# Optimization experiments

Measured on AMD Instinct MI355X. Metric: run time of the kernel, lower is better.

The kernel has to match this reference:

```python
import jax, jax.numpy as jnp
import numpy as np


def setup_inputs() -> dict:
    key = jax.random.key(0)
    ks = jax.random.split(key, 5)
    B, H, S, C, Dh = 2, 16, 2048, 2048, 64
    HID = H * Dh
    return {
        "q": jax.random.normal(ks[0], (B, H, S, Dh), dtype=jnp.float32),
        "k": jax.random.normal(ks[1], (B, H, C + S, Dh), dtype=jnp.float32),
        "v": jax.random.normal(ks[2], (B, H, C + S, Dh), dtype=jnp.float32),
        "memory_length": 256,
        "W": jax.random.normal(ks[3], (HID, HID), dtype=jnp.float32) / np.sqrt(HID),
        "b": jax.random.normal(ks[4], (HID,), dtype=jnp.float32) * 0.01,
    }


def _build_mask(S, KV, memory_length):
    # KV = CACHE_LEN + S; columns >= CACHE_LEN + memory_length are restricted.
    C = KV - S
    rows = jnp.arange(S)[:, None]          # query position in [0, S)
    cols = jnp.arange(KV)[None, :]         # key position in [0, KV)
    restricted = cols >= (C + memory_length)
    # memory rows (< memory_length) never see restricted cols;
    # other rows: strictly-upper-triangular masking (col - (C+mem) > row - mem)
    mem_row = rows < memory_length
    future = (cols - (C + memory_length)) > (rows - memory_length)
    return (restricted & (mem_row | future))  # bool [S, KV], True = masked


def reference(q, k, v, memory_length, W, b):
    B, H, S, Dh = q.shape
    KV = k.shape[2]
    HID = H * Dh
    scale = 1.0 / np.sqrt(Dh).astype(np.float32)
    scores = jnp.einsum('bhsd,bhtd->bhst', q, k) * scale   # [B,H,S,KV]
    mask2d = _build_mask(S, KV, memory_length)             # [S,KV] bool
    scores = jnp.where(mask2d[None, None], -jnp.inf, scores)
    attn_w = jax.nn.softmax(scores, axis=-1)
    attn = jnp.einsum('bhst,bhtd->bshd', attn_w, v).reshape(B, S, HID)
    out = attn @ W.T + b
    # torch module returns full [B,H,S,KV] float mask of 0/1
    mask_full = jnp.broadcast_to(mask2d.astype(q.dtype), (B, H, S, KV))
    return out, mask_full
```

## Files before the change

kernel.cpp:

```cpp
#include <hip/hip_runtime.h>
#include <hip/hip_bf16.h>
#include <math.h>

typedef __bf16 bf16;
typedef __bf16 bf16x4 __attribute__((ext_vector_type(4)));
typedef __bf16 bf16x8 __attribute__((ext_vector_type(8)));
typedef float f32x4 __attribute__((ext_vector_type(4)));

#define MFMA(a, b, c) __builtin_amdgcn_mfma_f32_16x16x32_bf16((a), (b), (c), 0, 0, 0)

constexpr int Bb  = 2;
constexpr int Hh  = 16;
constexpr int Ss  = 2048;
constexpr int KVv = 4096;
constexpr int Dd  = 64;
constexpr int Cc  = KVv - Ss;
constexpr int HID = Hh * Dd;

constexpr float QSCL = 0.125f * 1.44269504088896340736f;

constexpr size_t MASK_F4   = (size_t)Bb * Hh * Ss * KVv / 4;
constexpr size_t SCR_BYTES = 16777216ull + 16777216ull + 2097152ull + 8388608ull;
constexpr size_t M2_F4     = MASK_F4 - (2097152ull + 8388608ull) / 16;
constexpr size_t M1_F4     = 50000000;

__device__ __forceinline__ void write_mask_range(
    float* __restrict__ mout, int mem, size_t lo, size_t hi,
    int mblk, int nmblk, int tid, int nthr)
{
    const int R = Cc + mem;
    const size_t stride = (size_t)nmblk * nthr;
    for (size_t i = lo + (size_t)mblk * nthr + tid; i < hi; i += stride) {
        size_t flat = i * 4;
        int t = (int)(flat & (size_t)(KVv - 1));
        int s = (int)((flat >> 12) & (size_t)(Ss - 1));
        int thr = (s < mem) ? R : (s + Cc + 1);
        f32x4 vv;
        vv[0] = (float)(t >= thr);
        vv[1] = (float)(t + 1 >= thr);
        vv[2] = (float)(t + 2 >= thr);
        vv[3] = (float)(t + 3 >= thr);
        __builtin_nontemporal_store(vv, (f32x4*)(mout + flat));
    }
}

__global__ __launch_bounds__(256) void cvt_kernel(
    const float* __restrict__ K, const float* __restrict__ W,
    bf16* __restrict__ Kb, bf16* __restrict__ Wb)
{
    const size_t nK4 = (size_t)Bb * Hh * KVv * Dd / 4;
    const size_t nW4 = (size_t)HID * HID / 4;
    const size_t total = nK4 + nW4;
    const size_t stride = (size_t)gridDim.x * blockDim.x;
    for (size_t i = (size_t)blockIdx.x * blockDim.x + threadIdx.x; i < total; i += stride) {
        float4 x = (i < nK4) ? ((const float4*)K)[i] : ((const float4*)W)[i - nK4];
        bf16x4 t;
        t[0] = (bf16)x.x; t[1] = (bf16)x.y; t[2] = (bf16)x.z; t[3] = (bf16)x.w;
        if (i < nK4) ((bf16x4*)Kb)[i] = t;
        else         ((bf16x4*)Wb)[i - nK4] = t;
    }
}

__global__ __launch_bounds__(256) void vT_kernel(
    const float* __restrict__ V, bf16* __restrict__ Vt)
{
    __shared__ __align__(16) bf16 T[64][72];
    const int bh = blockIdx.y;
    const int t0 = blockIdx.x * 64;
    const int row = threadIdx.x >> 2;
    const int cg  = threadIdx.x & 3;

    const float* vb = V + (size_t)bh * KVv * Dd + (size_t)(t0 + row) * Dd + cg * 16;
    float4 x0 = ((const float4*)vb)[0];
    float4 x1 = ((const float4*)vb)[1];
    float4 x2 = ((const float4*)vb)[2];
    float4 x3 = ((const float4*)vb)[3];
    float xs[16] = {x0.x,x0.y,x0.z,x0.w, x1.x,x1.y,x1.z,x1.w,
                    x2.x,x2.y,x2.z,x2.w, x3.x,x3.y,x3.z,x3.w};
#pragma unroll
    for (int j = 0; j < 16; ++j)
        T[cg * 16 + j][row] = (bf16)xs[j];
    __syncthreads();

    const int d = row;
    bf16* o = Vt + (size_t)bh * Dd * KVv + (size_t)d * KVv + t0 + cg * 16;
    bf16x8 a0 = *(const bf16x8*)&T[d][cg * 16];
    bf16x8 a1 = *(const bf16x8*)&T[d][cg * 16 + 8];
    ((bf16x8*)o)[0] = a0;
    ((bf16x8*)o)[1] = a1;
}

template <bool MASKED>
__device__ __forceinline__ void kv_tile(
    int t0, const bf16* __restrict__ kb_p, const bf16* __restrict__ vt_p,
    const bf16x8 qa[2], const int thr[4], int tid, int lr, int lg,
    bf16 (*__restrict__ Klds)[72], bf16 (*__restrict__ Vlds)[72],
    bf16 (*__restrict__ Pw)[72], f32x4 acco[4], float lsum[4])
{
    {
        const int row = tid >> 3, c8 = tid & 7;
        bf16x8 kx = *(const bf16x8*)(kb_p + (size_t)(t0 + row) * Dd + c8 * 8);
        bf16x8 vx = *(const bf16x8*)(vt_p + (size_t)row * KVv + t0 + c8 * 8);
        *(bf16x8*)&Klds[row][c8 * 8] = kx;
        *(bf16x8*)&Vlds[row][c8 * 8] = vx;
    }
    __syncthreads();

    f32x4 accs[4];
#pragma unroll
    for (int kg = 0; kg < 4; ++kg) accs[kg] = (f32x4){0.f, 0.f, 0.f, 0.f};
    __builtin_amdgcn_s_setprio(1);
#pragma unroll
    for (int ks = 0; ks < 2; ++ks) {
#pragma unroll
        for (int kg = 0; kg < 4; ++kg) {
            bf16x8 kf = *(const bf16x8*)&Klds[kg * 16 + lr][ks * 32 + lg * 8];
            accs[kg] = MFMA(qa[ks], kf, accs[kg]);
        }
    }
    __builtin_amdgcn_s_setprio(0);

#pragma unroll
    for (int r = 0; r < 4; ++r) {
#pragma unroll
        for (int kg = 0; kg < 4; ++kg) {
            float sl = accs[kg][r];
            if (MASKED) {
                int tcol = t0 + kg * 16 + lr;
                sl = (tcol < thr[r]) ? sl : -1e30f;
            }
            accs[kg][r] = __builtin_amdgcn_exp2f(sl);
        }
        lsum[r] += (accs[0][r] + accs[1][r]) + (accs[2][r] + accs[3][r]);
#pragma unroll
        for (int kg = 0; kg < 4; ++kg)
            Pw[lg * 4 + r][kg * 16 + lr] = (bf16)accs[kg][r];
    }
    asm volatile("s_waitcnt lgkmcnt(0)" ::: "memory");

    __builtin_amdgcn_s_setprio(1);
#pragma unroll
    for (int ks = 0; ks < 2; ++ks) {
        bf16x8 pa = *(const bf16x8*)&Pw[lr][ks * 32 + lg * 8];
#pragma unroll
        for (int dg = 0; dg < 4; ++dg) {
            bf16x8 vf = *(const bf16x8*)&Vlds[dg * 16 + lr][ks * 32 + lg * 8];
            acco[dg] = MFMA(pa, vf, acco[dg]);
        }
    }
    __builtin_amdgcn_s_setprio(0);
    __syncthreads();
}

__global__ __launch_bounds__(512) void fused_attn_kernel(
    const float* __restrict__ q, const bf16* __restrict__ Kb,
    const bf16* __restrict__ Vtb, const int* __restrict__ memp,
    bf16* __restrict__ attnb, float* __restrict__ mout)
{
    __shared__ __align__(16) bf16 Klds[64][72];
    __shared__ __align__(16) bf16 Vlds[64][72];
    __shared__ __align__(16) bf16 Plds[8][16][72];

    const int fid = blockIdx.x;
    const int mem = *memp;
    if (fid >= 512) {
        write_mask_range(mout, mem, 0, M1_F4, fid - 512, gridDim.x - 512,
                         threadIdx.x, 512);
        return;
    }
    const int xcd = fid & 7;
    const int slot = fid >> 3;
    const int qblk = slot & 15;
    const int bh = (slot >> 4) * 8 + xcd;

    const int tid = threadIdx.x;
    const int w  = tid >> 6;
    const int l  = tid & 63;
    const int lr = l & 15;
    const int lg = l >> 4;
    const int q0 = qblk * 128;
    const int R = Cc + mem;

    const float* qp   = q   + (size_t)bh * Ss * Dd;
    const bf16*  kb_p = Kb  + (size_t)bh * KVv * Dd;
    const bf16*  vt_p = Vtb + (size_t)bh * Dd * KVv;

    const int qrow = q0 + w * 16 + lr;
    bf16x8 qa[2];
#pragma unroll
    for (int ks = 0; ks < 2; ++ks) {
        const float* p8 = qp + (size_t)qrow * Dd + ks * 32 + lg * 8;
        float4 x0 = *(const float4*)p8;
        float4 x1 = *(const float4*)(p8 + 4);
        bf16x8 a;
        a[0] = (bf16)(x0.x * QSCL); a[1] = (bf16)(x0.y * QSCL);
        a[2] = (bf16)(x0.z * QSCL); a[3] = (bf16)(x0.w * QSCL);
        a[4] = (bf16)(x1.x * QSCL); a[5] = (bf16)(x1.y * QSCL);
        a[6] = (bf16)(x1.z * QSCL); a[7] = (bf16)(x1.w * QSCL);
        qa[ks] = a;
    }

    int thr[4];
#pragma unroll
    for (int r = 0; r < 4; ++r) {
        int qabs = q0 + w * 16 + lg * 4 + r;
        thr[r] = (qabs < mem) ? R : (qabs + Cc + 1);
    }
    const int qmaxb = q0 + 127;
    int kv_end = (qmaxb < mem) ? R : (qmaxb + Cc + 1);
    if (kv_end > KVv) kv_end = KVv;
    int thr_min = (q0 < mem) ? R : (q0 + Cc + 1);
    int p1_end = thr_min & ~63;
    if (p1_end > kv_end) p1_end = kv_end;

    f32x4 acco[4];
#pragma unroll
    for (int dg = 0; dg < 4; ++dg) acco[dg] = (f32x4){0.f, 0.f, 0.f, 0.f};
    float lsum[4] = {0.f, 0.f, 0.f, 0.f};

    for (int t0 = 0; t0 < p1_end; t0 += 64)
        kv_tile<false>(t0, kb_p, vt_p, qa, thr, tid, lr, lg, Klds, Vlds, Plds[w], acco, lsum);
    for (int t0 = p1_end; t0 < kv_end; t0 += 64)
        kv_tile<true>(t0, kb_p, vt_p, qa, thr, tid, lr, lg, Klds, Vlds, Plds[w], acco, lsum);

    const int b = bh >> 4, h = bh & 15;
#pragma unroll
    for (int r = 0; r < 4; ++r) {
        float s = lsum[r];
        s += __shfl_xor(s, 1);
        s += __shfl_xor(s, 2);
        s += __shfl_xor(s, 4);
        s += __shfl_xor(s, 8);
        float inv = 1.f / s;
        int qabs = q0 + w * 16 + lg * 4 + r;
        bf16* dst = attnb + (size_t)(b * Ss + qabs) * HID + h * Dd;
#pragma unroll
        for (int dg = 0; dg < 4; ++dg)
            dst[dg * 16 + lr] = (bf16)(acco[dg][r] * inv);
    }
}

__global__ __launch_bounds__(256) void fused_proj_kernel(
    const bf16* __restrict__ A, const bf16* __restrict__ Wb,
    const float* __restrict__ bias, float* __restrict__ out,
    const int* __restrict__ memp, float* __restrict__ mout)
{
    __shared__ __align__(16) bf16 Alds[64][72];
    __shared__ __align__(16) bf16 Wlds[64][72];

    const int fid = blockIdx.x;
    if (fid >= 1024) {
        write_mask_range(mout, *memp, M1_F4, M2_F4, fid - 1024, gridDim.x - 1024,
                         threadIdx.x, 256);
        return;
    }
    const int xcd = fid & 7;
    const int slot = fid >> 3;
    const int o0 = ((slot & 1) * 8 + xcd) * 64;
    const int i0 = (slot >> 1) * 64;

    const int tid = threadIdx.x;
    const int w  = tid >> 6;
    const int l  = tid & 63;
    const int lr = l & 15;
    const int lg = l >> 4;

    f32x4 acc[4];
#pragma unroll
    for (int og = 0; og < 4; ++og) acc[og] = (f32x4){0.f, 0.f, 0.f, 0.f};

    for (int kc = 0; kc < HID; kc += 64) {
        const int row = tid >> 2, cg = tid & 3;
        bf16x8 a0 = ((const bf16x8*)(A  + (size_t)(i0 + row) * HID + kc + cg * 16))[0];
        bf16x8 a1 = ((const bf16x8*)(A  + (size_t)(i0 + row) * HID + kc + cg * 16))[1];
        bf16x8 w0 = ((const bf16x8*)(Wb + (size_t)(o0 + row) * HID + kc + cg * 16))[0];
        bf16x8 w1 = ((const bf16x8*)(Wb + (size_t)(o0 + row) * HID + kc + cg * 16))[1];
        *(bf16x8*)&Alds[row][cg * 16]     = a0;
        *(bf16x8*)&Alds[row][cg * 16 + 8] = a1;
        *(bf16x8*)&Wlds[row][cg * 16]     = w0;
        *(bf16x8*)&Wlds[row][cg * 16 + 8] = w1;
        __syncthreads();
        __builtin_amdgcn_s_setprio(1);
#pragma unroll
        for (int ks = 0; ks < 2; ++ks) {
            bf16x8 af = *(const bf16x8*)&Alds[w * 16 + lr][ks * 32 + lg * 8];
#pragma unroll
            for (int og = 0; og < 4; ++og) {
                bf16x8 wf = *(const bf16x8*)&Wlds[og * 16 + lr][ks * 32 + lg * 8];
                acc[og] = MFMA(af, wf, acc[og]);
            }
        }
        __builtin_amdgcn_s_setprio(0);
        __syncthreads();
    }

#pragma unroll
    for (int r = 0; r < 4; ++r) {
        int i = i0 + w * 16 + lg * 4 + r;
#pragma unroll
        for (int og = 0; og < 4; ++og) {
            int o = o0 + og * 16 + lr;
            __builtin_nontemporal_store(acc[og][r] + bias[o], &out[(size_t)i * HID + o]);
        }
    }
}

__global__ __launch_bounds__(256) void mask_tail_kernel(
    float* __restrict__ mout, const int* __restrict__ memp)
{
    write_mask_range(mout, *memp, M2_F4, MASK_F4, blockIdx.x, gridDim.x,
                     threadIdx.x, 256);
}

extern "C" void kernel_launch(void* const* d_in, const int* in_sizes, int n_in,
                              void* d_out, int out_size, void* d_ws, size_t ws_size,
                              hipStream_t stream)
{
    (void)in_sizes; (void)n_in; (void)out_size; (void)d_ws; (void)ws_size;
    const float* q    = (const float*)d_in[0];
    const float* k    = (const float*)d_in[1];
    const float* v    = (const float*)d_in[2];
    const int*   memp = (const int*)d_in[3];
    const float* W    = (const float*)d_in[4];
    const float* bias = (const float*)d_in[5];

    float* out     = (float*)d_out;
    float* maskout = out + (size_t)Bb * Ss * HID;

    char* scr = (char*)maskout + MASK_F4 * 16 - SCR_BYTES;
    bf16* Kbf   = (bf16*)scr;
    bf16* Vtb   = Kbf + (size_t)Bb * Hh * KVv * Dd;
    bf16* Wbf   = Vtb + (size_t)Bb * Hh * KVv * Dd;
    bf16* attnb = Wbf + (size_t)HID * HID;

    cvt_kernel<<<dim3(1024), 256, 0, stream>>>(k, W, Kbf, Wbf);
    vT_kernel<<<dim3(KVv / 64, Bb * Hh), 256, 0, stream>>>(v, Vtb);
    fused_attn_kernel<<<dim3(512 + 1024), 512, 0, stream>>>(q, Kbf, Vtb, memp, attnb, maskout);
    fused_proj_kernel<<<dim3(1024 + 512), 256, 0, stream>>>(attnb, Wbf, bias, out, memp, maskout);
    mask_tail_kernel<<<dim3(256), 256, 0, stream>>>(maskout, memp);
}
```

Before: 265.9 us.

## Double query rows per attention block, merge prep kernels, use workspace scratch

Each attention block now handles 256 query rows (two 16-row subtiles per wave), so every K/V tile staged in LDS is reused twice and half as many blocks reload K/V. The V transpose and the K/W bf16 conversion are merged into one prep launch. When the workspace is large enough, scratch moves into it, so the mask tail can be written by the projection kernel and the separate tail launch is dropped. The mask split point is also retuned. The cost is doubled register use for accumulators and Q fragments, and fewer attention blocks.

After: 301.9 us. 1.14x slower.

```diff
diff --git a/kernel.cpp b/kernel.cpp
--- a/kernel.cpp
+++ b/kernel.cpp
@@ -22,7 +22,7 @@
 constexpr size_t MASK_F4   = (size_t)Bb * Hh * Ss * KVv / 4;
 constexpr size_t SCR_BYTES = 16777216ull + 16777216ull + 2097152ull + 8388608ull;
 constexpr size_t M2_F4     = MASK_F4 - (2097152ull + 8388608ull) / 16;
-constexpr size_t M1_F4     = 50000000;
+constexpr size_t M1_F4     = 40000000;
 
 __device__ __forceinline__ void write_mask_range(
     float* __restrict__ mout, int mem, size_t lo, size_t hi,
@@ -44,15 +44,40 @@
     }
 }
 
-__global__ __launch_bounds__(256) void cvt_kernel(
+__global__ __launch_bounds__(256) void prep_kernel(
     const float* __restrict__ K, const float* __restrict__ W,
-    bf16* __restrict__ Kb, bf16* __restrict__ Wb)
-{
+    const float* __restrict__ V,
+    bf16* __restrict__ Kb, bf16* __restrict__ Wb, bf16* __restrict__ Vt)
+{
+    const int bid = blockIdx.x;
+    if (bid < 2048) {
+        __shared__ __align__(16) bf16 T[64][72];
+        const int bh = bid >> 6;
+        const int t0 = (bid & 63) * 64;
+        const int row = threadIdx.x >> 2;
+        const int cg  = threadIdx.x & 3;
+        const float* vb = V + (size_t)bh * KVv * Dd + (size_t)(t0 + row) * Dd + cg * 16;
+        float4 x0 = ((const float4*)vb)[0];
+        float4 x1 = ((const float4*)vb)[1];
+        float4 x2 = ((const float4*)vb)[2];
+        float4 x3 = ((const float4*)vb)[3];
+        float xs[16] = {x0.x,x0.y,x0.z,x0.w, x1.x,x1.y,x1.z,x1.w,
+                        x2.x,x2.y,x2.z,x2.w, x3.x,x3.y,x3.z,x3.w};
+#pragma unroll
+        for (int j = 0; j < 16; ++j)
+            T[cg * 16 + j][row] = (bf16)xs[j];
+        __syncthreads();
+        const int d = row;
+        bf16* o = Vt + (size_t)bh * Dd * KVv + (size_t)d * KVv + t0 + cg * 16;
+        ((bf16x8*)o)[0] = *(const bf16x8*)&T[d][cg * 16];
+        ((bf16x8*)o)[1] = *(const bf16x8*)&T[d][cg * 16 + 8];
+        return;
+    }
     const size_t nK4 = (size_t)Bb * Hh * KVv * Dd / 4;
     const size_t nW4 = (size_t)HID * HID / 4;
     const size_t total = nK4 + nW4;
-    const size_t stride = (size_t)gridDim.x * blockDim.x;
-    for (size_t i = (size_t)blockIdx.x * blockDim.x + threadIdx.x; i < total; i += stride) {
+    const size_t stride = (size_t)(gridDim.x - 2048) * 256;
+    for (size_t i = (size_t)(bid - 2048) * 256 + threadIdx.x; i < total; i += stride) {
         float4 x = (i < nK4) ? ((const float4*)K)[i] : ((const float4*)W)[i - nK4];
         bf16x4 t;
         t[0] = (bf16)x.x; t[1] = (bf16)x.y; t[2] = (bf16)x.z; t[3] = (bf16)x.w;
@@ -61,41 +86,12 @@
     }
 }
 
-__global__ __launch_bounds__(256) void vT_kernel(
-    const float* __restrict__ V, bf16* __restrict__ Vt)
-{
-    __shared__ __align__(16) bf16 T[64][72];
-    const int bh = blockIdx.y;
-    const int t0 = blockIdx.x * 64;
-    const int row = threadIdx.x >> 2;
-    const int cg  = threadIdx.x & 3;
-
-    const float* vb = V + (size_t)bh * KVv * Dd + (size_t)(t0 + row) * Dd + cg * 16;
-    float4 x0 = ((const float4*)vb)[0];
-    float4 x1 = ((const float4*)vb)[1];
-    float4 x2 = ((const float4*)vb)[2];
-    float4 x3 = ((const float4*)vb)[3];
-    float xs[16] = {x0.x,x0.y,x0.z,x0.w, x1.x,x1.y,x1.z,x1.w,
-                    x2.x,x2.y,x2.z,x2.w, x3.x,x3.y,x3.z,x3.w};
-#pragma unroll
-    for (int j = 0; j < 16; ++j)
-        T[cg * 16 + j][row] = (bf16)xs[j];
-    __syncthreads();
-
-    const int d = row;
-    bf16* o = Vt + (size_t)bh * Dd * KVv + (size_t)d * KVv + t0 + cg * 16;
-    bf16x8 a0 = *(const bf16x8*)&T[d][cg * 16];
-    bf16x8 a1 = *(const bf16x8*)&T[d][cg * 16 + 8];
-    ((bf16x8*)o)[0] = a0;
-    ((bf16x8*)o)[1] = a1;
-}
-
 template <bool MASKED>
 __device__ __forceinline__ void kv_tile(
     int t0, const bf16* __restrict__ kb_p, const bf16* __restrict__ vt_p,
-    const bf16x8 qa[2], const int thr[4], int tid, int lr, int lg,
+    const bf16x8 qa[2][2], const int thr[2][4], int tid, int lr, int lg,
     bf16 (*__restrict__ Klds)[72], bf16 (*__restrict__ Vlds)[72],
-    bf16 (*__restrict__ Pw)[72], f32x4 acco[4], float lsum[4])
+    bf16 (*__restrict__ Pw)[72], f32x4 acco[2][4], float lsum[2][4])
 {
     {
         const int row = tid >> 3, c8 = tid & 7;
@@ -106,49 +102,52 @@
     }
     __syncthreads();
 
-    f32x4 accs[4];
-#pragma unroll
-    for (int kg = 0; kg < 4; ++kg) accs[kg] = (f32x4){0.f, 0.f, 0.f, 0.f};
-    __builtin_amdgcn_s_setprio(1);
-#pragma unroll
-    for (int ks = 0; ks < 2; ++ks) {
-#pragma unroll
-        for (int kg = 0; kg < 4; ++kg) {
-            bf16x8 kf = *(const bf16x8*)&Klds[kg * 16 + lr][ks * 32 + lg * 8];
-            accs[kg] = MFMA(qa[ks], kf, accs[kg]);
-        }
-    }
-    __builtin_amdgcn_s_setprio(0);
-
-#pragma unroll
-    for (int r = 0; r < 4; ++r) {
-#pragma unroll
-        for (int kg = 0; kg < 4; ++kg) {
-            float sl = accs[kg][r];
-            if (MASKED) {
-                int tcol = t0 + kg * 16 + lr;
-                sl = (tcol < thr[r]) ? sl : -1e30f;
+#pragma unroll
+    for (int sq = 0; sq < 2; ++sq) {
+        f32x4 accs[4];
+#pragma unroll
+        for (int kg = 0; kg < 4; ++kg) accs[kg] = (f32x4){0.f, 0.f, 0.f, 0.f};
+        __builtin_amdgcn_s_setprio(1);
+#pragma unroll
+        for (int ks = 0; ks < 2; ++ks) {
+#pragma unroll
+            for (int kg = 0; kg < 4; ++kg) {
+                bf16x8 kf = *(const bf16x8*)&Klds[kg * 16 + lr][ks * 32 + lg * 8];
+                accs[kg] = MFMA(qa[sq][ks], kf, accs[kg]);
             }
-            accs[kg][r] = __builtin_amdgcn_exp2f(sl);
-        }
-        lsum[r] += (accs[0][r] + accs[1][r]) + (accs[2][r] + accs[3][r]);
-#pragma unroll
-        for (int kg = 0; kg < 4; ++kg)
-            Pw[lg * 4 + r][kg * 16 + lr] = (bf16)accs[kg][r];
-    }
-    asm volatile("s_waitcnt lgkmcnt(0)" ::: "memory");
-
-    __builtin_amdgcn_s_setprio(1);
-#pragma unroll
-    for (int ks = 0; ks < 2; ++ks) {
-        bf16x8 pa = *(const bf16x8*)&Pw[lr][ks * 32 + lg * 8];
-#pragma unroll
-        for (int dg = 0; dg < 4; ++dg) {
-            bf16x8 vf = *(const bf16x8*)&Vlds[dg * 16 + lr][ks * 32 + lg * 8];
-            acco[dg] = MFMA(pa, vf, acco[dg]);
-        }
-    }
-    __builtin_amdgcn_s_setprio(0);
+        }
+        __builtin_amdgcn_s_setprio(0);
+
+#pragma unroll
+        for (int r = 0; r < 4; ++r) {
+#pragma unroll
+            for (int kg = 0; kg < 4; ++kg) {
+                float sl = accs[kg][r];
+                if (MASKED) {
+                    int tcol = t0 + kg * 16 + lr;
+                    sl = (tcol < thr[sq][r]) ? sl : -1e30f;
+                }
+                accs[kg][r] = __builtin_amdgcn_exp2f(sl);
+            }
+            lsum[sq][r] += (accs[0][r] + accs[1][r]) + (accs[2][r] + accs[3][r]);
+#pragma unroll
+            for (int kg = 0; kg < 4; ++kg)
+                Pw[lg * 4 + r][kg * 16 + lr] = (bf16)accs[kg][r];
+        }
+        asm volatile("s_waitcnt lgkmcnt(0)" ::: "memory");
+
+        __builtin_amdgcn_s_setprio(1);
+#pragma unroll
+        for (int ks = 0; ks < 2; ++ks) {
+            bf16x8 pa = *(const bf16x8*)&Pw[lr][ks * 32 + lg * 8];
+#pragma unroll
+            for (int dg = 0; dg < 4; ++dg) {
+                bf16x8 vf = *(const bf16x8*)&Vlds[dg * 16 + lr][ks * 32 + lg * 8];
+                acco[sq][dg] = MFMA(pa, vf, acco[sq][dg]);
+            }
+        }
+        __builtin_amdgcn_s_setprio(0);
+    }
     __syncthreads();
 }
 
@@ -163,60 +162,65 @@
 
     const int fid = blockIdx.x;
     const int mem = *memp;
-    if (fid >= 512) {
-        write_mask_range(mout, mem, 0, M1_F4, fid - 512, gridDim.x - 512,
+    if (fid >= 256) {
+        write_mask_range(mout, mem, 0, M1_F4, fid - 256, gridDim.x - 256,
                          threadIdx.x, 512);
         return;
     }
     const int xcd = fid & 7;
     const int slot = fid >> 3;
-    const int qblk = slot & 15;
-    const int bh = (slot >> 4) * 8 + xcd;
+    const int qblk = slot & 7;
+    const int bh = (slot >> 3) * 8 + xcd;
 
     const int tid = threadIdx.x;
     const int w  = tid >> 6;
     const int l  = tid & 63;
     const int lr = l & 15;
     const int lg = l >> 4;
-    const int q0 = qblk * 128;
+    const int q0 = qblk * 256;
     const int R = Cc + mem;
 
     const float* qp   = q   + (size_t)bh * Ss * Dd;
     const bf16*  kb_p = Kb  + (size_t)bh * KVv * Dd;
     const bf16*  vt_p = Vtb + (size_t)bh * Dd * KVv;
 
-    const int qrow = q0 + w * 16 + lr;
-    bf16x8 qa[2];
-#pragma unroll
-    for (int ks = 0; ks < 2; ++ks) {
-        const float* p8 = qp + (size_t)qrow * Dd + ks * 32 + lg * 8;
-        float4 x0 = *(const float4*)p8;
-        float4 x1 = *(const float4*)(p8 + 4);
-        bf16x8 a;
-        a[0] = (bf16)(x0.x * QSCL); a[1] = (bf16)(x0.y * QSCL);
-        a[2] = (bf16)(x0.z * QSCL); a[3] = (bf16)(x0.w * QSCL);
-        a[4] = (bf16)(x1.x * QSCL); a[5] = (bf16)(x1.y * QSCL);
-        a[6] = (bf16)(x1.z * QSCL); a[7] = (bf16)(x1.w * QSCL);
-        qa[ks] = a;
-    }
-
-    int thr[4];
-#pragma unroll
-    for (int r = 0; r < 4; ++r) {
-        int qabs = q0 + w * 16 + lg * 4 + r;
-        thr[r] = (qabs < mem) ? R : (qabs + Cc + 1);
-    }
-    const int qmaxb = q0 + 127;
+    bf16x8 qa[2][2];
+    int thr[2][4];
+#pragma unroll
+    for (int sq = 0; sq < 2; ++sq) {
+        const int qrow = q0 + w * 32 + sq * 16 + lr;
+#pragma unroll
+        for (int ks = 0; ks < 2; ++ks) {
+            const float* p8 = qp + (size_t)qrow * Dd + ks * 32 + lg * 8;
+            float4 x0 = *(const float4*)p8;
+            float4 x1 = *(const float4*)(p8 + 4);
+            bf16x8 a;
+            a[0] = (bf16)(x0.x * QSCL); a[1] = (bf16)(x0.y * QSCL);
+            a[2] = (bf16)(x0.z * QSCL); a[3] = (bf16)(x0.w * QSCL);
+            a[4] = (bf16)(x1.x * QSCL); a[5] = (bf16)(x1.y * QSCL);
+            a[6] = (bf16)(x1.z * QSCL); a[7] = (bf16)(x1.w * QSCL);
+            qa[sq][ks] = a;
+        }
+#pragma unroll
+        for (int r = 0; r < 4; ++r) {
+            int qabs = q0 + w * 32 + sq * 16 + lg * 4 + r;
+            thr[sq][r] = (qabs < mem) ? R : (qabs + Cc + 1);
+        }
+    }
+
+    const int qmaxb = q0 + 255;
     int kv_end = (qmaxb < mem) ? R : (qmaxb + Cc + 1);
     if (kv_end > KVv) kv_end = KVv;
     int thr_min = (q0 < mem) ? R : (q0 + Cc + 1);
     int p1_end = thr_min & ~63;
     if (p1_end > kv_end) p1_end = kv_end;
 
-    f32x4 acco[4];
-#pragma unroll
-    for (int dg = 0; dg < 4; ++dg) acco[dg] = (f32x4){0.f, 0.f, 0.f, 0.f};
-    float lsum[4] = {0.f, 0.f, 0.f, 0.f};
+    f32x4 acco[2][4];
+#pragma unroll
+    for (int sq = 0; sq < 2; ++sq)
+#pragma unroll
+        for (int dg = 0; dg < 4; ++dg) acco[sq][dg] = (f32x4){0.f, 0.f, 0.f, 0.f};
+    float lsum[2][4] = {{0.f,0.f,0.f,0.f},{0.f,0.f,0.f,0.f}};
 
     for (int t0 = 0; t0 < p1_end; t0 += 64)
         kv_tile<false>(t0, kb_p, vt_p, qa, thr, tid, lr, lg, Klds, Vlds, Plds[w], acco, lsum);
@@ -225,32 +229,34 @@
 
     const int b = bh >> 4, h = bh & 15;
 #pragma unroll
+    for (int sq = 0; sq < 2; ++sq)
+#pragma unroll
     for (int r = 0; r < 4; ++r) {
-        float s = lsum[r];
+        float s = lsum[sq][r];
         s += __shfl_xor(s, 1);
         s += __shfl_xor(s, 2);
         s += __shfl_xor(s, 4);
         s += __shfl_xor(s, 8);
         float inv = 1.f / s;
-        int qabs = q0 + w * 16 + lg * 4 + r;
+        int qabs = q0 + w * 32 + sq * 16 + lg * 4 + r;
         bf16* dst = attnb + (size_t)(b * Ss + qabs) * HID + h * Dd;
 #pragma unroll
         for (int dg = 0; dg < 4; ++dg)
-            dst[dg * 16 + lr] = (bf16)(acco[dg][r] * inv);
+            dst[dg * 16 + lr] = (bf16)(acco[sq][dg][r] * inv);
     }
 }
 
 __global__ __launch_bounds__(256) void fused_proj_kernel(
     const bf16* __restrict__ A, const bf16* __restrict__ Wb,
     const float* __restrict__ bias, float* __restrict__ out,
-    const int* __restrict__ memp, float* __restrict__ mout)
+    const int* __restrict__ memp, float* __restrict__ mout, size_t mhi)
 {
     __shared__ __align__(16) bf16 Alds[64][72];
     __shared__ __align__(16) bf16 Wlds[64][72];
 
     const int fid = blockIdx.x;
     if (fid >= 1024) {
-        write_mask_range(mout, *memp, M1_F4, M2_F4, fid - 1024, gridDim.x - 1024,
+        write_mask_range(mout, *memp, M1_F4, mhi, fid - 1024, gridDim.x - 1024,
                          threadIdx.x, 256);
         return;
     }
@@ -316,7 +322,7 @@
                               void* d_out, int out_size, void* d_ws, size_t ws_size,
                               hipStream_t stream)
 {
-    (void)in_sizes; (void)n_in; (void)out_size; (void)d_ws; (void)ws_size;
+    (void)in_sizes; (void)n_in; (void)out_size;
     const float* q    = (const float*)d_in[0];
     const float* k    = (const float*)d_in[1];
     const float* v    = (const float*)d_in[2];
@@ -327,15 +333,19 @@
     float* out     = (float*)d_out;
     float* maskout = out + (size_t)Bb * Ss * HID;
 
-    char* scr = (char*)maskout + MASK_F4 * 16 - SCR_BYTES;
+    const bool use_ws = ws_size >= SCR_BYTES;
+    char* scr = use_ws ? (char*)d_ws
+                       : (char*)maskout + MASK_F4 * 16 - SCR_BYTES;
     bf16* Kbf   = (bf16*)scr;
     bf16* Vtb   = Kbf + (size_t)Bb * Hh * KVv * Dd;
     bf16* Wbf   = Vtb + (size_t)Bb * Hh * KVv * Dd;
     bf16* attnb = Wbf + (size_t)HID * HID;
 
-    cvt_kernel<<<dim3(1024), 256, 0, stream>>>(k, W, Kbf, Wbf);
-    vT_kernel<<<dim3(KVv / 64, Bb * Hh), 256, 0, stream>>>(v, Vtb);
-    fused_attn_kernel<<<dim3(512 + 1024), 512, 0, stream>>>(q, Kbf, Vtb, memp, attnb, maskout);
-    fused_proj_kernel<<<dim3(1024 + 512), 256, 0, stream>>>(attnb, Wbf, bias, out, memp, maskout);
-    mask_tail_kernel<<<dim3(256), 256, 0, stream>>>(maskout, memp);
-}
+    const size_t mhi = use_ws ? MASK_F4 : M2_F4;
+
+    prep_kernel<<<dim3(2048 + 1024), 256, 0, stream>>>(k, W, v, Kbf, Wbf, Vtb);
+    fused_attn_kernel<<<dim3(256 + 1024), 512, 0, stream>>>(q, Kbf, Vtb, memp, attnb, maskout);
+    fused_proj_kernel<<<dim3(1024 + 512), 256, 0, stream>>>(attnb, Wbf, bias, out, memp, maskout, mhi);
+    if (!use_ws)
+        mask_tail_kernel<<<dim3(256), 256, 0, stream>>>(maskout, memp);
+}
```
